# Optimization experiments

Hardware: AMD Instinct MI355X
Metric: run time of the kernel (lower is better)

Reference implementation:

```python
import jax, jax.numpy as jnp
import numpy as np

B, N_SRC, N_NGH = 2048, 1, 64
FEAT = EDGE = TIME = POS = 128
D_MODEL = FEAT + EDGE + TIME + POS  # 512
N_HEAD = 4
D_K = D_MODEL // N_HEAD  # 128
LN_EPS = 1e-5


def setup_inputs() -> dict:
    key = jax.random.key(0)
    ks = jax.random.split(key, 24)
    s = 0.05
    inp = {
        "src":   jax.random.normal(ks[0], (B, N_SRC, FEAT), jnp.float32),
        "src_t": jax.random.normal(ks[1], (B, N_SRC, TIME), jnp.float32),
        "src_p": jax.random.normal(ks[2], (B, N_SRC, POS), jnp.float32),
        "seq":   jax.random.normal(ks[3], (B, N_NGH, FEAT), jnp.float32),
        "seq_t": jax.random.normal(ks[4], (B, N_NGH, TIME), jnp.float32),
        "seq_e": jax.random.normal(ks[5], (B, N_NGH, EDGE), jnp.float32),
        "seq_p": jax.random.normal(ks[6], (B, N_NGH, POS), jnp.float32),
        "mask":  jax.random.randint(ks[7], (B, N_SRC, N_NGH), 0, 2).astype(bool),
        # MapBasedMultiHeadAttention params (Linear stored as [in, out])
        "Wq": jax.random.normal(ks[8],  (D_MODEL, N_HEAD * D_K), jnp.float32) * s,
        "Wk": jax.random.normal(ks[9],  (D_MODEL, N_HEAD * D_K), jnp.float32) * s,
        "Wv": jax.random.normal(ks[10], (D_MODEL, N_HEAD * D_K), jnp.float32) * s,
        "w_map": jax.random.normal(ks[11], (2 * D_K,), jnp.float32) * s,  # Linear(2*d_k, 1, bias=False)
        "fc_w": jax.random.normal(ks[12], (N_HEAD * D_K, D_MODEL), jnp.float32) * s,
        "fc_b": jnp.zeros((D_MODEL,), jnp.float32),
        "ln_g": jnp.ones((D_MODEL,), jnp.float32),
        "ln_b": jnp.zeros((D_MODEL,), jnp.float32),
        # MergeLayer(model_dim, feat_dim, feat_dim, feat_dim)
        "fc1_w": jax.random.normal(ks[13], (D_MODEL + FEAT, FEAT), jnp.float32) * s,
        "fc1_b": jnp.zeros((FEAT,), jnp.float32),
        "fc2_w": jax.random.normal(ks[14], (FEAT, FEAT), jnp.float32) * s,
        "fc2_b": jnp.zeros((FEAT,), jnp.float32),
    }
    return inp


def _forward(src, src_t, src_p, seq, seq_t, seq_e, seq_p, mask,
             Wq, Wk, Wv, w_map, fc_w, fc_b, ln_g, ln_b,
             fc1_w, fc1_b, fc2_w, fc2_b):
    b, ns, feat = src.shape
    nn = seq.shape[1]
    dk = w_map.shape[0] // 2
    h = Wq.shape[1] // dk

    # AttnModel: queries get zero edge features
    src_e = jnp.zeros((b, ns, seq_e.shape[-1]), src.dtype)
    q_in = jnp.concatenate([src, src_e, src_t, src_p], axis=-1)  # [B, Ns, D]
    k_in = jnp.concatenate([seq, seq_e, seq_t, seq_p], axis=-1)  # [B, Nn, D]

    qh = (q_in @ Wq).reshape(b, ns, h, dk)  # [B, Ns, H, dk]
    kh = (k_in @ Wk).reshape(b, nn, h, dk)  # [B, Nn, H, dk]
    vh = (k_in @ Wv).reshape(b, nn, h, dk)  # [B, Nn, H, dv]

    # weight_map(cat([q, k], -1)) == q . w_map[:dk] + k . w_map[dk:]
    # (linear in the concat -> decomposes into an outer sum; same math,
    #  avoids materializing the [H*B, Ns, Nn, 2*dk] concat tensor)
    q_score = jnp.einsum('bqhd,d->bhq', qh, w_map[:dk])
    k_score = jnp.einsum('bkhd,d->bhk', kh, w_map[dk:])
    attn = q_score[..., None] + k_score[:, :, None, :]  # [B, H, Ns, Nn]

    attn = jnp.where(mask[:, None, :, :], jnp.float32(-1e10), attn)
    attn = jax.nn.softmax(attn, axis=-1)

    out = jnp.einsum('bhqk,bkhd->bqhd', attn, vh).reshape(b, ns, h * dk)
    out = jax.nn.leaky_relu(out @ fc_w + fc_b, negative_slope=0.2)

    # residual + layernorm over d_model
    out = out + q_in
    mu = jnp.mean(out, axis=-1, keepdims=True)
    var = jnp.var(out, axis=-1, keepdims=True)
    out = (out - mu) * jax.lax.rsqrt(var + LN_EPS) * ln_g + ln_b

    # MergeLayer (non_linear=True)
    x = jnp.concatenate([out, src], axis=-1)  # [B, Ns, D+feat]
    z = jax.nn.relu(x @ fc1_w + fc1_b) @ fc2_w + fc2_b  # [B, Ns, feat]
    return z, attn


def reference(src, src_t, src_p, seq, seq_t, seq_e, seq_p, mask,
              Wq, Wk, Wv, w_map, fc_w, fc_b, ln_g, ln_b,
              fc1_w, fc1_b, fc2_w, fc2_b):
    return _forward(src, src_t, src_p, seq, seq_t, seq_e, seq_p, mask,
                    Wq, Wk, Wv, w_map, fc_w, fc_b, ln_g, ln_b,
                    fc1_w, fc1_b, fc2_w, fc2_b)
```

## Files before the change

### kernel.cpp

```cpp
#include <hip/hip_runtime.h>
#include <stdint.h>


#define DEV static __device__ __forceinline__

typedef __attribute__((ext_vector_type(8))) short short8;
typedef __attribute__((ext_vector_type(4))) float floatx4;

DEV unsigned short f2bf(float f) {
    unsigned int x; __builtin_memcpy(&x, &f, 4);
    unsigned int r = (x + 0x7fffu + ((x >> 16) & 1u)) >> 16;
    return (unsigned short)r;
}

__global__ __launch_bounds__(256) void prep(const float* __restrict__ Wk,
                                            const float* __restrict__ w_map,
                                            const float* __restrict__ Wv,
                                            const float* __restrict__ fc_w,
                                            float* __restrict__ wk_eff,
                                            unsigned short* __restrict__ Gt) {
    const int t = threadIdx.x;
    if (blockIdx.x >= 256) {
        int n = (blockIdx.x - 256) * 256 + t;
        int h = n >> 9, c = n & 511;
        const float* wrow = Wk + (size_t)c * 512 + h * 128;
        const float* wm = w_map + 128;
        float acc = 0.f;
        #pragma unroll 8
        for (int d = 0; d < 128; d += 4) {
            float4 a = *(const float4*)(wrow + d);
            float4 b = *(const float4*)(wm + d);
            acc += a.x * b.x + a.y * b.y + a.z * b.z + a.w * b.w;
        }
        wk_eff[h * 512 + c] = acc;
        return;
    }
    __shared__ float wv[8 * 128];
    int r0 = blockIdx.x * 8;
    int h = r0 >> 9, c0 = r0 & 511;
    {
        int idx = t * 4;
        int i = idx >> 7, d = idx & 127;
        *(float4*)&wv[idx] = *(const float4*)(Wv + (size_t)(c0 + i) * 512 + h * 128 + d);
    }
    __syncthreads();
    float acc[8][2];
    #pragma unroll
    for (int i = 0; i < 8; i++) { acc[i][0] = 0.f; acc[i][1] = 0.f; }
    const float* fw = fc_w + (size_t)(h * 128) * 512 + t;
    for (int d = 0; d < 128; d++) {
        float w0 = fw[(size_t)d * 512];
        float w1 = fw[(size_t)d * 512 + 256];
        #pragma unroll
        for (int i = 0; i < 8; i++) {
            float a = wv[i * 128 + d];
            acc[i][0] += a * w0;
            acc[i][1] += a * w1;
        }
    }
    uint4 o0, o1;
    o0.x = ((unsigned int)f2bf(acc[1][0]) << 16) | f2bf(acc[0][0]);
    o0.y = ((unsigned int)f2bf(acc[3][0]) << 16) | f2bf(acc[2][0]);
    o0.z = ((unsigned int)f2bf(acc[5][0]) << 16) | f2bf(acc[4][0]);
    o0.w = ((unsigned int)f2bf(acc[7][0]) << 16) | f2bf(acc[6][0]);
    o1.x = ((unsigned int)f2bf(acc[1][1]) << 16) | f2bf(acc[0][1]);
    o1.y = ((unsigned int)f2bf(acc[3][1]) << 16) | f2bf(acc[2][1]);
    o1.z = ((unsigned int)f2bf(acc[5][1]) << 16) | f2bf(acc[4][1]);
    o1.w = ((unsigned int)f2bf(acc[7][1]) << 16) | f2bf(acc[6][1]);
    *(uint4*)(Gt + (size_t)t * 2048 + r0)         = o0;
    *(uint4*)(Gt + (size_t)(t + 256) * 2048 + r0) = o1;
}

__global__ __launch_bounds__(256) void attn2(const float* __restrict__ seq,
                                             const float* __restrict__ seq_t,
                                             const float* __restrict__ seq_e,
                                             const float* __restrict__ seq_p,
                                             const int* __restrict__ mask,
                                             const float* __restrict__ wk_eff,
                                             float* __restrict__ attn_out,
                                             unsigned short* __restrict__ ctxb) {
    __shared__ float cbuf[4][2048];
    __shared__ float tbuf[4][4];
    const int b = blockIdx.x, t = threadIdx.x, w = t >> 6, l = t & 63;
    const int sg = l >> 4;
    const float* base = (sg == 0 ? seq : sg == 1 ? seq_e : sg == 2 ? seq_t : seq_p)
                        + (size_t)b * 8192 + (l & 15) * 8;
    float4 wka[4], wkb[4];
    #pragma unroll
    for (int h = 0; h < 4; h++) {
        wka[h] = *(const float4*)(wk_eff + h * 512 + l * 8);
        wkb[h] = *(const float4*)(wk_eff + h * 512 + l * 8 + 4);
    }
    const int ml = mask[b * 64 + l];

    const float* p = base + w * 16 * 128;
    float4 ra = *(const float4*)p;
    float4 rb = *(const float4*)(p + 4);
    float c8[4][8];
    #pragma unroll
    for (int h = 0; h < 4; h++)
        #pragma unroll
        for (int j = 0; j < 8; j++) c8[h][j] = 0.f;
    float tot[4] = {0.f, 0.f, 0.f, 0.f};
    float em = 0.f;

    for (int kr = 0; kr < 16; kr++) {
        float4 na = ra, nb = rb;
        if (kr < 15) {
            const float* pn = p + (kr + 1) * 128;
            na = *(const float4*)pn;
            nb = *(const float4*)(pn + 4);
        }
        float s0 = ra.x*wka[0].x + ra.y*wka[0].y + ra.z*wka[0].z + ra.w*wka[0].w
                 + rb.x*wkb[0].x + rb.y*wkb[0].y + rb.z*wkb[0].z + rb.w*wkb[0].w;
        float s1 = ra.x*wka[1].x + ra.y*wka[1].y + ra.z*wka[1].z + ra.w*wka[1].w
                 + rb.x*wkb[1].x + rb.y*wkb[1].y + rb.z*wkb[1].z + rb.w*wkb[1].w;
        float s2 = ra.x*wka[2].x + ra.y*wka[2].y + ra.z*wka[2].z + ra.w*wka[2].w
                 + rb.x*wkb[2].x + rb.y*wkb[2].y + rb.z*wkb[2].z + rb.w*wkb[2].w;
        float s3 = ra.x*wka[3].x + ra.y*wka[3].y + ra.z*wka[3].z + ra.w*wka[3].w
                 + rb.x*wkb[3].x + rb.y*wkb[3].y + rb.z*wkb[3].z + rb.w*wkb[3].w;
        #pragma unroll
        for (int m = 1; m < 64; m <<= 1) {
            s0 += __shfl_xor(s0, m, 64);
            s1 += __shfl_xor(s1, m, 64);
            s2 += __shfl_xor(s2, m, 64);
            s3 += __shfl_xor(s3, m, 64);
        }
        const int mk = __shfl(ml, w * 16 + kr, 64);
        float e0 = mk ? 0.f : __expf(s0);
        float e1 = mk ? 0.f : __expf(s1);
        float e2 = mk ? 0.f : __expf(s2);
        float e3 = mk ? 0.f : __expf(s3);
        tot[0] += e0; tot[1] += e1; tot[2] += e2; tot[3] += e3;
        float eh = sg == 0 ? e0 : sg == 1 ? e1 : sg == 2 ? e2 : e3;
        if ((l & 15) == kr) em = eh;
        float rv[8] = {ra.x, ra.y, ra.z, ra.w, rb.x, rb.y, rb.z, rb.w};
        float ee[4] = {e0, e1, e2, e3};
        #pragma unroll
        for (int h = 0; h < 4; h++)
            #pragma unroll
            for (int j = 0; j < 8; j++) c8[h][j] += ee[h] * rv[j];
        ra = na; rb = nb;
    }

    #pragma unroll
    for (int h = 0; h < 4; h++) {
        float4 u0 = {c8[h][0], c8[h][1], c8[h][2], c8[h][3]};
        float4 u1 = {c8[h][4], c8[h][5], c8[h][6], c8[h][7]};
        *(float4*)&cbuf[w][h * 512 + l * 8]     = u0;
        *(float4*)&cbuf[w][h * 512 + l * 8 + 4] = u1;
    }
    if (l == 0) {
        tbuf[w][0] = tot[0]; tbuf[w][1] = tot[1];
        tbuf[w][2] = tot[2]; tbuf[w][3] = tot[3];
    }
    __syncthreads();

    const int i0 = t * 8;
    float4 u0 = *(const float4*)&cbuf[0][i0];
    float4 u1 = *(const float4*)&cbuf[0][i0 + 4];
    #pragma unroll
    for (int w2 = 1; w2 < 4; w2++) {
        float4 v0 = *(const float4*)&cbuf[w2][i0];
        float4 v1 = *(const float4*)&cbuf[w2][i0 + 4];
        u0.x += v0.x; u0.y += v0.y; u0.z += v0.z; u0.w += v0.w;
        u1.x += v1.x; u1.y += v1.y; u1.z += v1.z; u1.w += v1.w;
    }
    const int hh = t >> 6;
    float ts = tbuf[0][hh] + tbuf[1][hh] + tbuf[2][hh] + tbuf[3][hh];
    float rt = 1.f / ts;
    uint4 o;
    o.x = ((unsigned int)f2bf(u0.y * rt) << 16) | f2bf(u0.x * rt);
    o.y = ((unsigned int)f2bf(u0.w * rt) << 16) | f2bf(u0.z * rt);
    o.z = ((unsigned int)f2bf(u1.y * rt) << 16) | f2bf(u1.x * rt);
    o.w = ((unsigned int)f2bf(u1.w * rt) << 16) | f2bf(u1.z * rt);
    *(uint4*)(ctxb + (size_t)b * 2048 + i0) = o;

    float tl = tbuf[0][sg] + tbuf[1][sg] + tbuf[2][sg] + tbuf[3][sg];
    attn_out[b * 256 + sg * 64 + w * 16 + (l & 15)] = em / tl;
}

__global__ __launch_bounds__(256) void gemm2(const unsigned short* __restrict__ A,
                                             const unsigned short* __restrict__ Bt,
                                             float* __restrict__ C) {
    __shared__ __align__(16) unsigned short As[64 * 64];
    __shared__ __align__(16) unsigned short Bs[64 * 64];
    const int t = threadIdx.x;
    const int m0 = blockIdx.x * 64, n0 = blockIdx.y * 64;
    const int w = t >> 6, lane = t & 63, quad = lane >> 4, l16 = lane & 15;
    const int wm = w >> 1, wn = w & 1;
    const int sr0 = t >> 3, g = t & 7, sr1 = sr0 + 32;
    const unsigned short* pa0 = A  + (size_t)(m0 + sr0) * 2048 + g * 8;
    const unsigned short* pa1 = A  + (size_t)(m0 + sr1) * 2048 + g * 8;
    const unsigned short* pb0 = Bt + (size_t)(n0 + sr0) * 2048 + g * 8;
    const unsigned short* pb1 = Bt + (size_t)(n0 + sr1) * 2048 + g * 8;
    const int da0 = sr0 * 64 + ((g ^ (sr0 & 7)) * 8);
    const int da1 = sr1 * 64 + ((g ^ (sr1 & 7)) * 8);
    floatx4 acc00 = {0.f,0.f,0.f,0.f}, acc01 = {0.f,0.f,0.f,0.f};
    floatx4 acc10 = {0.f,0.f,0.f,0.f}, acc11 = {0.f,0.f,0.f,0.f};
    uint4 va0 = *(const uint4*)pa0, va1 = *(const uint4*)pa1;
    uint4 vb0 = *(const uint4*)pb0, vb1 = *(const uint4*)pb1;
    const int ra = wm * 32 + l16, rb = wn * 32 + l16;
    for (int k0 = 0; k0 < 2048; k0 += 64) {
        *(uint4*)&As[da0] = va0; *(uint4*)&As[da1] = va1;
        *(uint4*)&Bs[da0] = vb0; *(uint4*)&Bs[da1] = vb1;
        __syncthreads();
        if (k0 < 2048 - 64) {
            va0 = *(const uint4*)(pa0 + k0 + 64);
            va1 = *(const uint4*)(pa1 + k0 + 64);
            vb0 = *(const uint4*)(pb0 + k0 + 64);
            vb1 = *(const uint4*)(pb1 + k0 + 64);
        }
        #pragma unroll
        for (int ks = 0; ks < 2; ks++) {
            int grp = ks * 4 + quad;
            short8 a0 = *(const short8*)&As[ra * 64 + ((grp ^ (ra & 7)) * 8)];
            short8 a1 = *(const short8*)&As[(ra + 16) * 64 + ((grp ^ (ra & 7)) * 8)];
            short8 b0 = *(const short8*)&Bs[rb * 64 + ((grp ^ (rb & 7)) * 8)];
            short8 b1 = *(const short8*)&Bs[(rb + 16) * 64 + ((grp ^ (rb & 7)) * 8)];
            acc00 = __builtin_amdgcn_mfma_f32_16x16x32_bf16(a0, b0, acc00, 0, 0, 0);
            acc01 = __builtin_amdgcn_mfma_f32_16x16x32_bf16(a0, b1, acc01, 0, 0, 0);
            acc10 = __builtin_amdgcn_mfma_f32_16x16x32_bf16(a1, b0, acc10, 0, 0, 0);
            acc11 = __builtin_amdgcn_mfma_f32_16x16x32_bf16(a1, b1, acc11, 0, 0, 0);
        }
        __syncthreads();
    }
    float* c0 = C + (size_t)(m0 + wm * 32) * 512 + n0 + wn * 32;
    #pragma unroll
    for (int i = 0; i < 4; i++) {
        int r = quad * 4 + i;
        c0[(size_t)r * 512 + l16]             = acc00[i];
        c0[(size_t)r * 512 + l16 + 16]        = acc01[i];
        c0[(size_t)(r + 16) * 512 + l16]      = acc10[i];
        c0[(size_t)(r + 16) * 512 + l16 + 16] = acc11[i];
    }
}

__global__ __launch_bounds__(256) void epilogue(const float* __restrict__ out_pre,
                                                const float* __restrict__ src,
                                                const float* __restrict__ src_t,
                                                const float* __restrict__ src_p,
                                                const float* __restrict__ fc_b,
                                                const float* __restrict__ ln_g,
                                                const float* __restrict__ ln_b,
                                                const float* __restrict__ fc1_w,
                                                const float* __restrict__ fc1_b,
                                                const float* __restrict__ fc2_w,
                                                const float* __restrict__ fc2_b,
                                                float* __restrict__ z_out) {
    __shared__ float oln[8][512];
    __shared__ float t1p[2][8][128];
    __shared__ float t1[8][128];
    const int t = threadIdx.x;
    const int b0 = blockIdx.x * 8;
    const int w = t >> 6, lane = t & 63;

    for (int e = 0; e < 2; e++) {
        int bb = w * 2 + e;
        int b = b0 + bb;
        float vals[8];
        float sum = 0.f, ssq = 0.f;
        #pragma unroll
        for (int i = 0; i < 8; i++) {
            int c = lane + (i << 6);
            float v = out_pre[(size_t)b * 512 + c] + fc_b[c];
            v = (v > 0.f) ? v : 0.2f * v;
            float q;
            int seg = c >> 7;
            if (seg == 0)      q = src[b * 128 + c];
            else if (seg == 1) q = 0.f;
            else if (seg == 2) q = src_t[b * 128 + c - 256];
            else               q = src_p[b * 128 + c - 384];
            v += q;
            vals[i] = v;
            sum += v;
            ssq += v * v;
        }
        #pragma unroll
        for (int m = 32; m; m >>= 1) {
            sum += __shfl_xor(sum, m, 64);
            ssq += __shfl_xor(ssq, m, 64);
        }
        float mu = sum * (1.f / 512.f);
        float var = ssq * (1.f / 512.f) - mu * mu;
        float rstd = rsqrtf(var + 1e-5f);
        #pragma unroll
        for (int i = 0; i < 8; i++) {
            int c = lane + (i << 6);
            oln[bb][c] = (vals[i] - mu) * rstd * ln_g[c] + ln_b[c];
        }
    }
    __syncthreads();

    {
        int j = t & 127, hf = t >> 7;
        float acc[8];
        #pragma unroll
        for (int bb = 0; bb < 8; bb++) acc[bb] = (hf == 0) ? fc1_b[j] : 0.f;
        int i0 = hf * 320;
        for (int ic = 0; ic < 320; ic += 4) {
            int i = i0 + ic;
            float w0 = fc1_w[(size_t)(i + 0) * 128 + j];
            float w1 = fc1_w[(size_t)(i + 1) * 128 + j];
            float w2 = fc1_w[(size_t)(i + 2) * 128 + j];
            float w3 = fc1_w[(size_t)(i + 3) * 128 + j];
            #pragma unroll
            for (int bb = 0; bb < 8; bb++) {
                float4 x;
                if (i < 512) x = *(const float4*)&oln[bb][i];
                else         x = *(const float4*)(src + (size_t)(b0 + bb) * 128 + (i - 512));
                acc[bb] += x.x * w0 + x.y * w1 + x.z * w2 + x.w * w3;
            }
        }
        #pragma unroll
        for (int bb = 0; bb < 8; bb++) t1p[hf][bb][j] = acc[bb];
    }
    __syncthreads();
    {
        int j = t & 127, g = t >> 7;
        #pragma unroll
        for (int e = 0; e < 4; e++) {
            int bb = g * 4 + e;
            t1[bb][j] = fmaxf(t1p[0][bb][j] + t1p[1][bb][j], 0.f);
        }
    }
    __syncthreads();

    {
        int j = t & 127, g = t >> 7;
        float acc[4];
        #pragma unroll
        for (int e = 0; e < 4; e++) acc[e] = fc2_b[j];
        for (int i = 0; i < 128; i++) {
            float w2 = fc2_w[(size_t)i * 128 + j];
            #pragma unroll
            for (int e = 0; e < 4; e++) acc[e] += t1[g * 4 + e][i] * w2;
        }
        #pragma unroll
        for (int e = 0; e < 4; e++)
            z_out[(size_t)(b0 + g * 4 + e) * 128 + j] = acc[e];
    }
}

extern "C" void kernel_launch(void* const* d_in, const int* in_sizes, int n_in,
                              void* d_out, int out_size, void* d_ws, size_t ws_size,
                              hipStream_t stream) {
    const float* src   = (const float*)d_in[0];
    const float* src_t = (const float*)d_in[1];
    const float* src_p = (const float*)d_in[2];
    const float* seq   = (const float*)d_in[3];
    const float* seq_t = (const float*)d_in[4];
    const float* seq_e = (const float*)d_in[5];
    const float* seq_p = (const float*)d_in[6];
    const int*   mask  = (const int*)d_in[7];
    const float* Wk    = (const float*)d_in[9];
    const float* Wv    = (const float*)d_in[10];
    const float* w_map = (const float*)d_in[11];
    const float* fc_w  = (const float*)d_in[12];
    const float* fc_b  = (const float*)d_in[13];
    const float* ln_g  = (const float*)d_in[14];
    const float* ln_b  = (const float*)d_in[15];
    const float* fc1_w = (const float*)d_in[16];
    const float* fc1_b = (const float*)d_in[17];
    const float* fc2_w = (const float*)d_in[18];
    const float* fc2_b = (const float*)d_in[19];

    float* z_out    = (float*)d_out;
    float* attn_out = (float*)d_out + 2048 * 128;

    char* ws = (char*)d_ws;
    float*          wk_eff  = (float*)ws;
    unsigned short* Gt      = (unsigned short*)(ws + 16384);
    unsigned short* ctxb    = (unsigned short*)(ws + 16384 + (2u << 20));
    float*          out_pre = (float*)(ws + 16384 + (2u << 20) + (8u << 20));

    hipLaunchKernelGGL(prep, dim3(264), dim3(256), 0, stream,
                       Wk, w_map, Wv, fc_w, wk_eff, Gt);
    hipLaunchKernelGGL(attn2, dim3(2048), dim3(256), 0, stream,
                       seq, seq_t, seq_e, seq_p, mask, wk_eff, attn_out, ctxb);
    hipLaunchKernelGGL(gemm2, dim3(32, 8), dim3(256), 0, stream, ctxb, Gt, out_pre);
    hipLaunchKernelGGL(epilogue, dim3(256), dim3(256), 0, stream, out_pre,
                       src, src_t, src_p, fc_b, ln_g, ln_b,
                       fc1_w, fc1_b, fc2_w, fc2_b, z_out);
}
```

Measured before the change: 381.0 us.

## Rewrite attention kernel with bf16 MFMA and shrink gemm and epilogue tiles

The attention kernel now stages the neighbor features into swizzled bf16 shared memory, computes key scores and the context with MFMA instead of FP32 FMAs plus wave shuffles, and stores wk_eff pre-laid out as MFMA fragments. Separately, the gemm tile shrinks from 64 to 32 rows and the epilogue handles 4 rows per block instead of 8, doubling grid sizes to improve occupancy. Scores are now computed from bf16-rounded inputs, which loses some precision, and the context MFMA wastes most lanes since only 4 heads are active.

```diff
diff --git a/kernel.cpp b/kernel.cpp
--- a/kernel.cpp
+++ b/kernel.cpp
@@ -9,15 +9,19 @@
 
 DEV unsigned short f2bf(float f) {
     unsigned int x; __builtin_memcpy(&x, &f, 4);
-    unsigned int r = (x + 0x7fffu + ((x >> 16) & 1u)) >> 16;
-    return (unsigned short)r;
+    return (unsigned short)((x + 0x7fffu + ((x >> 16) & 1u)) >> 16);
+}
+DEV unsigned int pk2(float hi, float lo) {
+    unsigned int a, b;
+    __builtin_memcpy(&a, &hi, 4); __builtin_memcpy(&b, &lo, 4);
+    return __builtin_amdgcn_perm(a, b, 0x07060302u);
 }
 
 __global__ __launch_bounds__(256) void prep(const float* __restrict__ Wk,
                                             const float* __restrict__ w_map,
                                             const float* __restrict__ Wv,
                                             const float* __restrict__ fc_w,
-                                            float* __restrict__ wk_eff,
+                                            unsigned short* __restrict__ wkfrag,
                                             unsigned short* __restrict__ Gt) {
     const int t = threadIdx.x;
     if (blockIdx.x >= 256) {
@@ -32,7 +36,10 @@
             float4 b = *(const float4*)(wm + d);
             acc += a.x * b.x + a.y * b.y + a.z * b.z + a.w * b.w;
         }
-        wk_eff[h * 512 + c] = acc;
+        int kk = c >> 5, quad = (c >> 3) & 3, j = c & 7;
+        unsigned short* p = wkfrag + (((kk * 4 + quad) * 16) + h) * 8 + j;
+        p[0] = f2bf(acc);
+        p[32] = 0; p[64] = 0; p[96] = 0;
         return;
     }
     __shared__ float wv[8 * 128];
@@ -71,193 +78,186 @@
     *(uint4*)(Gt + (size_t)(t + 256) * 2048 + r0) = o1;
 }
 
-__global__ __launch_bounds__(256) void attn2(const float* __restrict__ seq,
+__global__ __launch_bounds__(256) void attn3(const float* __restrict__ seq,
                                              const float* __restrict__ seq_t,
                                              const float* __restrict__ seq_e,
                                              const float* __restrict__ seq_p,
                                              const int* __restrict__ mask,
-                                             const float* __restrict__ wk_eff,
+                                             const unsigned short* __restrict__ wkfrag,
                                              float* __restrict__ attn_out,
                                              unsigned short* __restrict__ ctxb) {
-    __shared__ float cbuf[4][2048];
-    __shared__ float tbuf[4][4];
-    const int b = blockIdx.x, t = threadIdx.x, w = t >> 6, l = t & 63;
-    const int sg = l >> 4;
-    const float* base = (sg == 0 ? seq : sg == 1 ? seq_e : sg == 2 ? seq_t : seq_p)
-                        + (size_t)b * 8192 + (l & 15) * 8;
-    float4 wka[4], wkb[4];
-    #pragma unroll
-    for (int h = 0; h < 4; h++) {
-        wka[h] = *(const float4*)(wk_eff + h * 512 + l * 8);
-        wkb[h] = *(const float4*)(wk_eff + h * 512 + l * 8 + 4);
-    }
-    const int ml = mask[b * 64 + l];
-
-    const float* p = base + w * 16 * 128;
-    float4 ra = *(const float4*)p;
-    float4 rb = *(const float4*)(p + 4);
-    float c8[4][8];
-    #pragma unroll
-    for (int h = 0; h < 4; h++)
-        #pragma unroll
-        for (int j = 0; j < 8; j++) c8[h][j] = 0.f;
-    float tot[4] = {0.f, 0.f, 0.f, 0.f};
-    float em = 0.f;
-
-    for (int kr = 0; kr < 16; kr++) {
-        float4 na = ra, nb = rb;
-        if (kr < 15) {
-            const float* pn = p + (kr + 1) * 128;
-            na = *(const float4*)pn;
-            nb = *(const float4*)(pn + 4);
-        }
-        float s0 = ra.x*wka[0].x + ra.y*wka[0].y + ra.z*wka[0].z + ra.w*wka[0].w
-                 + rb.x*wkb[0].x + rb.y*wkb[0].y + rb.z*wkb[0].z + rb.w*wkb[0].w;
-        float s1 = ra.x*wka[1].x + ra.y*wka[1].y + ra.z*wka[1].z + ra.w*wka[1].w
-                 + rb.x*wkb[1].x + rb.y*wkb[1].y + rb.z*wkb[1].z + rb.w*wkb[1].w;
-        float s2 = ra.x*wka[2].x + ra.y*wka[2].y + ra.z*wka[2].z + ra.w*wka[2].w
-                 + rb.x*wkb[2].x + rb.y*wkb[2].y + rb.z*wkb[2].z + rb.w*wkb[2].w;
-        float s3 = ra.x*wka[3].x + ra.y*wka[3].y + ra.z*wka[3].z + ra.w*wka[3].w
-                 + rb.x*wkb[3].x + rb.y*wkb[3].y + rb.z*wkb[3].z + rb.w*wkb[3].w;
-        #pragma unroll
-        for (int m = 1; m < 64; m <<= 1) {
-            s0 += __shfl_xor(s0, m, 64);
-            s1 += __shfl_xor(s1, m, 64);
-            s2 += __shfl_xor(s2, m, 64);
-            s3 += __shfl_xor(s3, m, 64);
-        }
-        const int mk = __shfl(ml, w * 16 + kr, 64);
-        float e0 = mk ? 0.f : __expf(s0);
-        float e1 = mk ? 0.f : __expf(s1);
-        float e2 = mk ? 0.f : __expf(s2);
-        float e3 = mk ? 0.f : __expf(s3);
-        tot[0] += e0; tot[1] += e1; tot[2] += e2; tot[3] += e3;
-        float eh = sg == 0 ? e0 : sg == 1 ? e1 : sg == 2 ? e2 : e3;
-        if ((l & 15) == kr) em = eh;
-        float rv[8] = {ra.x, ra.y, ra.z, ra.w, rb.x, rb.y, rb.z, rb.w};
-        float ee[4] = {e0, e1, e2, e3};
-        #pragma unroll
-        for (int h = 0; h < 4; h++)
+    __shared__ __align__(16) unsigned short kinb[64 * 512];
+    __shared__ float sd[64 * 5];
+    __shared__ __align__(16) float pb[256];
+    __shared__ __align__(16) float cb[4 * 512];
+    const int b = blockIdx.x, t = threadIdx.x;
+    const int w = t >> 6, l16 = t & 15, quad = (t >> 4) & 3;
+
+    #pragma unroll 8
+    for (int step = 0; step < 16; step++) {
+        int g = step * 256 + t;
+        int row = g >> 6, gcol = g & 63;
+        int seg = gcol >> 4;
+        const float* p = (seg == 0 ? seq : seg == 1 ? seq_e : seg == 2 ? seq_t : seq_p)
+                         + (size_t)b * 8192 + row * 128 + (gcol & 15) * 8;
+        float4 v0 = *(const float4*)p;
+        float4 v1 = *(const float4*)(p + 4);
+        uint4 pk;
+        pk.x = pk2(v0.y, v0.x); pk.y = pk2(v0.w, v0.z);
+        pk.z = pk2(v1.y, v1.x); pk.w = pk2(v1.w, v1.z);
+        int ps = gcol ^ (row & 7) ^ ((row >> 3) & 7);
+        *(uint4*)&kinb[row * 512 + ps * 8] = pk;
+    }
+    __syncthreads();
+
+    short8 wkf[16];
+    #pragma unroll
+    for (int kk = 0; kk < 16; kk++)
+        wkf[kk] = *(const short8*)(wkfrag + (((kk * 4 + quad) * 16) + l16) * 8);
+    floatx4 sacc = {0.f, 0.f, 0.f, 0.f};
+    const int srow = w * 16 + l16;
+    const int rs = (srow & 7) ^ ((srow >> 3) & 7);
+    #pragma unroll
+    for (int kk = 0; kk < 16; kk++) {
+        short8 af = *(const short8*)&kinb[srow * 512 + ((kk * 4 + quad) ^ rs) * 8];
+        sacc = __builtin_amdgcn_mfma_f32_16x16x32_bf16(af, wkf[kk], sacc, 0, 0, 0);
+    }
+    if (l16 < 4) {
+        #pragma unroll
+        for (int r = 0; r < 4; r++) sd[(w * 16 + quad * 4 + r) * 5 + l16] = sacc[r];
+    }
+    __syncthreads();
+
+    {
+        int row = t & 63, head = t >> 6;
+        float s = sd[row * 5 + head];
+        float e = mask[b * 64 + row] ? 0.f : __expf(s);
+        float sum = e;
+        #pragma unroll
+        for (int m = 32; m; m >>= 1) sum += __shfl_xor(sum, m, 64);
+        float pr = e / sum;
+        attn_out[b * 256 + t] = pr;
+        pb[t] = pr;
+    }
+    __syncthreads();
+
+    floatx4 cacc[8];
+    #pragma unroll
+    for (int nt = 0; nt < 8; nt++) cacc[nt] = (floatx4){0.f, 0.f, 0.f, 0.f};
+    #pragma unroll
+    for (int s = 0; s < 2; s++) {
+        short8 afr = {0, 0, 0, 0, 0, 0, 0, 0};
+        if (l16 < 4) {
+            const float* pp = pb + l16 * 64 + s * 32 + quad * 8;
+            float4 u0 = *(const float4*)pp;
+            float4 u1 = *(const float4*)(pp + 4);
+            uint4 tmp;
+            tmp.x = pk2(u0.y, u0.x); tmp.y = pk2(u0.w, u0.z);
+            tmp.z = pk2(u1.y, u1.x); tmp.w = pk2(u1.w, u1.z);
+            __builtin_memcpy(&afr, &tmp, 16);
+        }
+        const int sq = s * 4 + quad;
+        #pragma unroll
+        for (int nt = 0; nt < 8; nt++) {
+            const int c = w * 128 + nt * 16 + l16;
+            const int gc = c >> 3, co = c & 7;
+            short8 bfr;
             #pragma unroll
-            for (int j = 0; j < 8; j++) c8[h][j] += ee[h] * rv[j];
-        ra = na; rb = nb;
-    }
-
-    #pragma unroll
-    for (int h = 0; h < 4; h++) {
-        float4 u0 = {c8[h][0], c8[h][1], c8[h][2], c8[h][3]};
-        float4 u1 = {c8[h][4], c8[h][5], c8[h][6], c8[h][7]};
-        *(float4*)&cbuf[w][h * 512 + l * 8]     = u0;
-        *(float4*)&cbuf[w][h * 512 + l * 8 + 4] = u1;
-    }
-    if (l == 0) {
-        tbuf[w][0] = tot[0]; tbuf[w][1] = tot[1];
-        tbuf[w][2] = tot[2]; tbuf[w][3] = tot[3];
-    }
-    __syncthreads();
-
-    const int i0 = t * 8;
-    float4 u0 = *(const float4*)&cbuf[0][i0];
-    float4 u1 = *(const float4*)&cbuf[0][i0 + 4];
-    #pragma unroll
-    for (int w2 = 1; w2 < 4; w2++) {
-        float4 v0 = *(const float4*)&cbuf[w2][i0];
-        float4 v1 = *(const float4*)&cbuf[w2][i0 + 4];
-        u0.x += v0.x; u0.y += v0.y; u0.z += v0.z; u0.w += v0.w;
-        u1.x += v1.x; u1.y += v1.y; u1.z += v1.z; u1.w += v1.w;
-    }
-    const int hh = t >> 6;
-    float ts = tbuf[0][hh] + tbuf[1][hh] + tbuf[2][hh] + tbuf[3][hh];
-    float rt = 1.f / ts;
-    uint4 o;
-    o.x = ((unsigned int)f2bf(u0.y * rt) << 16) | f2bf(u0.x * rt);
-    o.y = ((unsigned int)f2bf(u0.w * rt) << 16) | f2bf(u0.z * rt);
-    o.z = ((unsigned int)f2bf(u1.y * rt) << 16) | f2bf(u1.x * rt);
-    o.w = ((unsigned int)f2bf(u1.w * rt) << 16) | f2bf(u1.z * rt);
-    *(uint4*)(ctxb + (size_t)b * 2048 + i0) = o;
-
-    float tl = tbuf[0][sg] + tbuf[1][sg] + tbuf[2][sg] + tbuf[3][sg];
-    attn_out[b * 256 + sg * 64 + w * 16 + (l & 15)] = em / tl;
-}
-
-__global__ __launch_bounds__(256) void gemm2(const unsigned short* __restrict__ A,
+            for (int j = 0; j < 8; j++) {
+                int r = s * 32 + quad * 8 + j;
+                bfr[j] = (short)kinb[r * 512 + (gc ^ j ^ sq) * 8 + co];
+            }
+            cacc[nt] = __builtin_amdgcn_mfma_f32_16x16x32_bf16(afr, bfr, cacc[nt], 0, 0, 0);
+        }
+    }
+    if (quad == 0) {
+        #pragma unroll
+        for (int nt = 0; nt < 8; nt++) {
+            int c = w * 128 + nt * 16 + l16;
+            #pragma unroll
+            for (int r = 0; r < 4; r++) cb[r * 512 + c] = cacc[nt][r];
+        }
+    }
+    __syncthreads();
+    {
+        const float* pp = cb + t * 8;
+        float4 u0 = *(const float4*)pp, u1 = *(const float4*)(pp + 4);
+        uint4 pk;
+        pk.x = pk2(u0.y, u0.x); pk.y = pk2(u0.w, u0.z);
+        pk.z = pk2(u1.y, u1.x); pk.w = pk2(u1.w, u1.z);
+        *(uint4*)(ctxb + (size_t)b * 2048 + t * 8) = pk;
+    }
+}
+
+__global__ __launch_bounds__(256) void gemm3(const unsigned short* __restrict__ A,
                                              const unsigned short* __restrict__ Bt,
                                              float* __restrict__ C) {
-    __shared__ __align__(16) unsigned short As[64 * 64];
+    __shared__ __align__(16) unsigned short As[32 * 64];
     __shared__ __align__(16) unsigned short Bs[64 * 64];
     const int t = threadIdx.x;
-    const int m0 = blockIdx.x * 64, n0 = blockIdx.y * 64;
+    const int m0 = blockIdx.x * 32, n0 = blockIdx.y * 64;
     const int w = t >> 6, lane = t & 63, quad = lane >> 4, l16 = lane & 15;
     const int wm = w >> 1, wn = w & 1;
-    const int sr0 = t >> 3, g = t & 7, sr1 = sr0 + 32;
-    const unsigned short* pa0 = A  + (size_t)(m0 + sr0) * 2048 + g * 8;
-    const unsigned short* pa1 = A  + (size_t)(m0 + sr1) * 2048 + g * 8;
-    const unsigned short* pb0 = Bt + (size_t)(n0 + sr0) * 2048 + g * 8;
-    const unsigned short* pb1 = Bt + (size_t)(n0 + sr1) * 2048 + g * 8;
-    const int da0 = sr0 * 64 + ((g ^ (sr0 & 7)) * 8);
-    const int da1 = sr1 * 64 + ((g ^ (sr1 & 7)) * 8);
-    floatx4 acc00 = {0.f,0.f,0.f,0.f}, acc01 = {0.f,0.f,0.f,0.f};
-    floatx4 acc10 = {0.f,0.f,0.f,0.f}, acc11 = {0.f,0.f,0.f,0.f};
-    uint4 va0 = *(const uint4*)pa0, va1 = *(const uint4*)pa1;
-    uint4 vb0 = *(const uint4*)pb0, vb1 = *(const uint4*)pb1;
-    const int ra = wm * 32 + l16, rb = wn * 32 + l16;
+    const int ar = t >> 3, g = t & 7;
+    const int br0 = t >> 3, br1 = br0 + 32;
+    const unsigned short* pa  = A  + (size_t)(m0 + ar) * 2048 + g * 8;
+    const unsigned short* pb0 = Bt + (size_t)(n0 + br0) * 2048 + g * 8;
+    const unsigned short* pb1 = Bt + (size_t)(n0 + br1) * 2048 + g * 8;
+    const int da  = ar * 64 + (g ^ (ar & 7)) * 8;
+    const int db0 = br0 * 64 + (g ^ (br0 & 7)) * 8;
+    const int db1 = br1 * 64 + (g ^ (br1 & 7)) * 8;
+    floatx4 acc0 = {0.f,0.f,0.f,0.f}, acc1 = {0.f,0.f,0.f,0.f};
+    uint4 va = *(const uint4*)pa, vb0 = *(const uint4*)pb0, vb1 = *(const uint4*)pb1;
+    const int ra = wm * 16 + l16, rb = wn * 32 + l16;
     for (int k0 = 0; k0 < 2048; k0 += 64) {
-        *(uint4*)&As[da0] = va0; *(uint4*)&As[da1] = va1;
-        *(uint4*)&Bs[da0] = vb0; *(uint4*)&Bs[da1] = vb1;
+        *(uint4*)&As[da] = va; *(uint4*)&Bs[db0] = vb0; *(uint4*)&Bs[db1] = vb1;
         __syncthreads();
-        if (k0 < 2048 - 64) {
-            va0 = *(const uint4*)(pa0 + k0 + 64);
-            va1 = *(const uint4*)(pa1 + k0 + 64);
+        if (k0 < 1984) {
+            va  = *(const uint4*)(pa  + k0 + 64);
             vb0 = *(const uint4*)(pb0 + k0 + 64);
             vb1 = *(const uint4*)(pb1 + k0 + 64);
         }
         #pragma unroll
         for (int ks = 0; ks < 2; ks++) {
             int grp = ks * 4 + quad;
-            short8 a0 = *(const short8*)&As[ra * 64 + ((grp ^ (ra & 7)) * 8)];
-            short8 a1 = *(const short8*)&As[(ra + 16) * 64 + ((grp ^ (ra & 7)) * 8)];
+            short8 a  = *(const short8*)&As[ra * 64 + ((grp ^ (ra & 7)) * 8)];
             short8 b0 = *(const short8*)&Bs[rb * 64 + ((grp ^ (rb & 7)) * 8)];
             short8 b1 = *(const short8*)&Bs[(rb + 16) * 64 + ((grp ^ (rb & 7)) * 8)];
-            acc00 = __builtin_amdgcn_mfma_f32_16x16x32_bf16(a0, b0, acc00, 0, 0, 0);
-            acc01 = __builtin_amdgcn_mfma_f32_16x16x32_bf16(a0, b1, acc01, 0, 0, 0);
-            acc10 = __builtin_amdgcn_mfma_f32_16x16x32_bf16(a1, b0, acc10, 0, 0, 0);
-            acc11 = __builtin_amdgcn_mfma_f32_16x16x32_bf16(a1, b1, acc11, 0, 0, 0);
+            acc0 = __builtin_amdgcn_mfma_f32_16x16x32_bf16(a, b0, acc0, 0, 0, 0);
+            acc1 = __builtin_amdgcn_mfma_f32_16x16x32_bf16(a, b1, acc1, 0, 0, 0);
         }
         __syncthreads();
     }
-    float* c0 = C + (size_t)(m0 + wm * 32) * 512 + n0 + wn * 32;
-    #pragma unroll
-    for (int i = 0; i < 4; i++) {
-        int r = quad * 4 + i;
-        c0[(size_t)r * 512 + l16]             = acc00[i];
-        c0[(size_t)r * 512 + l16 + 16]        = acc01[i];
-        c0[(size_t)(r + 16) * 512 + l16]      = acc10[i];
-        c0[(size_t)(r + 16) * 512 + l16 + 16] = acc11[i];
-    }
-}
-
-__global__ __launch_bounds__(256) void epilogue(const float* __restrict__ out_pre,
-                                                const float* __restrict__ src,
-                                                const float* __restrict__ src_t,
-                                                const float* __restrict__ src_p,
-                                                const float* __restrict__ fc_b,
-                                                const float* __restrict__ ln_g,
-                                                const float* __restrict__ ln_b,
-                                                const float* __restrict__ fc1_w,
-                                                const float* __restrict__ fc1_b,
-                                                const float* __restrict__ fc2_w,
-                                                const float* __restrict__ fc2_b,
-                                                float* __restrict__ z_out) {
-    __shared__ float oln[8][512];
-    __shared__ float t1p[2][8][128];
-    __shared__ float t1[8][128];
+    float* cp = C + (size_t)(m0 + wm * 16) * 512 + n0 + wn * 32;
+    #pragma unroll
+    for (int r = 0; r < 4; r++) {
+        int rr = quad * 4 + r;
+        cp[(size_t)rr * 512 + l16]      = acc0[r];
+        cp[(size_t)rr * 512 + l16 + 16] = acc1[r];
+    }
+}
+
+__global__ __launch_bounds__(256) void epilogue4(const float* __restrict__ out_pre,
+                                                 const float* __restrict__ src,
+                                                 const float* __restrict__ src_t,
+                                                 const float* __restrict__ src_p,
+                                                 const float* __restrict__ fc_b,
+                                                 const float* __restrict__ ln_g,
+                                                 const float* __restrict__ ln_b,
+                                                 const float* __restrict__ fc1_w,
+                                                 const float* __restrict__ fc1_b,
+                                                 const float* __restrict__ fc2_w,
+                                                 const float* __restrict__ fc2_b,
+                                                 float* __restrict__ z_out) {
+    __shared__ float oln[4][512];
+    __shared__ float t1p[2][4][128];
+    __shared__ float t1[4][128];
     const int t = threadIdx.x;
-    const int b0 = blockIdx.x * 8;
+    const int b0 = blockIdx.x * 4;
     const int w = t >> 6, lane = t & 63;
 
-    for (int e = 0; e < 2; e++) {
-        int bb = w * 2 + e;
-        int b = b0 + bb;
+    {
+        int b = b0 + w;
         float vals[8];
         float sum = 0.f, ssq = 0.f;
         #pragma unroll
@@ -273,8 +273,7 @@
             else               q = src_p[b * 128 + c - 384];
             v += q;
             vals[i] = v;
-            sum += v;
-            ssq += v * v;
+            sum += v; ssq += v * v;
         }
         #pragma unroll
         for (int m = 32; m; m >>= 1) {
@@ -287,16 +286,16 @@
         #pragma unroll
         for (int i = 0; i < 8; i++) {
             int c = lane + (i << 6);
-            oln[bb][c] = (vals[i] - mu) * rstd * ln_g[c] + ln_b[c];
+            oln[w][c] = (vals[i] - mu) * rstd * ln_g[c] + ln_b[c];
         }
     }
     __syncthreads();
 
     {
         int j = t & 127, hf = t >> 7;
-        float acc[8];
-        #pragma unroll
-        for (int bb = 0; bb < 8; bb++) acc[bb] = (hf == 0) ? fc1_b[j] : 0.f;
+        float acc[4];
+        #pragma unroll
+        for (int bb = 0; bb < 4; bb++) acc[bb] = (hf == 0) ? fc1_b[j] : 0.f;
         int i0 = hf * 320;
         for (int ic = 0; ic < 320; ic += 4) {
             int i = i0 + ic;
@@ -305,7 +304,7 @@
             float w2 = fc1_w[(size_t)(i + 2) * 128 + j];
             float w3 = fc1_w[(size_t)(i + 3) * 128 + j];
             #pragma unroll
-            for (int bb = 0; bb < 8; bb++) {
+            for (int bb = 0; bb < 4; bb++) {
                 float4 x;
                 if (i < 512) x = *(const float4*)&oln[bb][i];
                 else         x = *(const float4*)(src + (size_t)(b0 + bb) * 128 + (i - 512));
@@ -313,32 +312,31 @@
             }
         }
         #pragma unroll
-        for (int bb = 0; bb < 8; bb++) t1p[hf][bb][j] = acc[bb];
+        for (int bb = 0; bb < 4; bb++) t1p[hf][bb][j] = acc[bb];
     }
     __syncthreads();
     {
         int j = t & 127, g = t >> 7;
         #pragma unroll
-        for (int e = 0; e < 4; e++) {
-            int bb = g * 4 + e;
+        for (int e = 0; e < 2; e++) {
+            int bb = g * 2 + e;
             t1[bb][j] = fmaxf(t1p[0][bb][j] + t1p[1][bb][j], 0.f);
         }
     }
     __syncthreads();
-
     {
         int j = t & 127, g = t >> 7;
-        float acc[4];
-        #pragma unroll
-        for (int e = 0; e < 4; e++) acc[e] = fc2_b[j];
+        float acc[2];
+        #pragma unroll
+        for (int e = 0; e < 2; e++) acc[e] = fc2_b[j];
         for (int i = 0; i < 128; i++) {
             float w2 = fc2_w[(size_t)i * 128 + j];
             #pragma unroll
-            for (int e = 0; e < 4; e++) acc[e] += t1[g * 4 + e][i] * w2;
-        }
-        #pragma unroll
-        for (int e = 0; e < 4; e++)
-            z_out[(size_t)(b0 + g * 4 + e) * 128 + j] = acc[e];
+            for (int e = 0; e < 2; e++) acc[e] += t1[g * 2 + e][i] * w2;
+        }
+        #pragma unroll
+        for (int e = 0; e < 2; e++)
+            z_out[(size_t)(b0 + g * 2 + e) * 128 + j] = acc[e];
     }
 }
 
@@ -369,17 +367,17 @@
     float* attn_out = (float*)d_out + 2048 * 128;
 
     char* ws = (char*)d_ws;
-    float*          wk_eff  = (float*)ws;
-    unsigned short* Gt      = (unsigned short*)(ws + 16384);
-    unsigned short* ctxb    = (unsigned short*)(ws + 16384 + (2u << 20));
-    float*          out_pre = (float*)(ws + 16384 + (2u << 20) + (8u << 20));
+    unsigned short* wkfrag  = (unsigned short*)ws;
+    unsigned short* Gt      = (unsigned short*)(ws + 65536);
+    unsigned short* ctxb    = (unsigned short*)(ws + 65536 + (2u << 20));
+    float*          out_pre = (float*)(ws + 65536 + (10u << 20));
 
     hipLaunchKernelGGL(prep, dim3(264), dim3(256), 0, stream,
-                       Wk, w_map, Wv, fc_w, wk_eff, Gt);
-    hipLaunchKernelGGL(attn2, dim3(2048), dim3(256), 0, stream,
-                       seq, seq_t, seq_e, seq_p, mask, wk_eff, attn_out, ctxb);
-    hipLaunchKernelGGL(gemm2, dim3(32, 8), dim3(256), 0, stream, ctxb, Gt, out_pre);
-    hipLaunchKernelGGL(epilogue, dim3(256), dim3(256), 0, stream, out_pre,
+                       Wk, w_map, Wv, fc_w, wkfrag, Gt);
+    hipLaunchKernelGGL(attn3, dim3(2048), dim3(256), 0, stream,
+                       seq, seq_t, seq_e, seq_p, mask, wkfrag, attn_out, ctxb);
+    hipLaunchKernelGGL(gemm3, dim3(64, 8), dim3(256), 0, stream, ctxb, Gt, out_pre);
+    hipLaunchKernelGGL(epilogue4, dim3(512), dim3(256), 0, stream, out_pre,
                        src, src_t, src_p, fc_b, ln_g, ln_b,
                        fc1_w, fc1_b, fc2_w, fc2_b, z_out);
 }
```

Measured after the change: 361.7 us. -5.1%, faster.
